# Kernel optimization log

Hardware: AMD Instinct MI355X
Metric: run time of the kernel (lower is better)

## Reference

```python
import jax, jax.numpy as jnp
import numpy as np
from jax import lax

N = 2048
B = 8
CH = 10
START = 1
STOP = 65


def setup_inputs() -> dict:
    key = jax.random.key(0)
    ks = jax.random.split(key, 13)

    def g(k, s):
        return jax.random.normal(k, s, jnp.float32) * 0.05

    return {
        "x": jax.random.normal(ks[0], (B, 1, N, N), jnp.float32),
        "wl": g(ks[1], (CH // 2, 1, 3, N)), "bl": g(ks[2], (CH // 2,)),
        "wr": g(ks[3], (CH // 2, 1, N, 3)), "br": g(ks[4], (CH // 2,)),
        "wA": g(ks[5], (CH, CH, 3)), "bA": g(ks[6], (CH,)),
        "wB": g(ks[7], (CH, CH, 3)), "bB": g(ks[8], (CH,)),  # shared by layers 2&3 (torch list aliasing)
        "wT": g(ks[9], (CH, CH, 3)), "bT": g(ks[10], (CH,)),
        "wm": g(ks[11], (2, CH, 1)), "bm": g(ks[12], (2,)),
        "start": START, "stop": STOP,
    }


def _conv1d(h, w, b, pad):
    y = lax.conv_general_dilated(h, w, (1,), [(pad, pad)], dimension_numbers=("NCH", "OIH", "NCH"))
    return y + b[None, :, None]


def _forward(x, wl, bl, wr, br, wA, bA, wB, bB, wT, bT, wm, bm, start, stop):
    n = x.shape[-1]
    # scan_left: Conv2d kernel (3, n), padding (1, 0) -> (B, 5, n, 1) -> squeeze
    left_ = lax.conv_general_dilated(x, wl, (1, 1), [(1, 1), (0, 0)], dimension_numbers=("NCHW", "OIHW", "NCHW"))
    left_ = left_[..., 0] + bl[None, :, None]
    # scan_right: Conv2d kernel (n, 3), padding (0, 1) -> (B, 5, 1, n) -> squeeze
    right_ = lax.conv_general_dilated(x, wr, (1, 1), [(0, 0), (1, 1)], dimension_numbers=("NCHW", "OIHW", "NCHW"))
    right_ = right_[:, :, 0, :] + br[None, :, None]
    lr = jnp.concatenate([left_, right_], axis=1)  # (B, 10, n)
    h = jax.nn.relu(_conv1d(lr, wA, bA, 1))
    h = jax.nn.relu(_conv1d(h, wB, bB, 1))  # same weights twice: torch [conv, relu]*2 aliasing
    h = jax.nn.relu(_conv1d(h, wB, bB, 1))
    # ConvTranspose1d(k=3, stride=1, pad=1) == Conv1d with transposed, spatially-flipped kernel, pad=1
    wTc = jnp.flip(jnp.swapaxes(wT, 0, 1), -1)
    for _ in range(3):
        h = jax.nn.relu(_conv1d(h, wTc, bT, 1))
    m = jax.nn.sigmoid(_conv1d(h, wm, bm, 0))  # (B, 2, n)
    left, right = m[:, 0, :], m[:, 1, :]
    xs = x[:, 0]  # (B, n, n)
    preds = []
    for d in range(start, stop):  # static diagonal indices
        curr = jnp.exp(jnp.diagonal(xs, offset=d, axis1=1, axis2=2))  # (B, n-d)
        mass_in = curr[:, 1:] * right[:, 1:n - d] + curr[:, :-1] * left[:, d:n - 1]
        mass_out = right[:, 0:n - d - 1] + left[:, d + 1:n]
        p = jnp.log(mass_in / mass_out)
        preds.append(p - jnp.mean(p))  # scalar mean over batch+positions, as torch.mean
    return jnp.concatenate(preds, axis=1)  # ragged preds concatenated: (B, sum(n-d-1))


def reference(x, wl, bl, wr, br, wA, bA, wB, bB, wT, bT, wm, bm, start, stop):
    return _forward(x, wl, bl, wr, br, wA, bA, wB, bB, wT, bT, wm, bm, start, stop)
```

## Files before the change

kernel.cpp:

```cpp
#include <hip/hip_runtime.h>
#include <hip/hip_bf16.h>

#define NN 2048
#define BB 8
#define TROW 128928

typedef __attribute__((ext_vector_type(8))) short bf16x8;
typedef __attribute__((ext_vector_type(4))) float f32x4;

__device__ __forceinline__ short f2bf(float f) {
    unsigned u = __float_as_uint(f);
    unsigned r = (u + 0x7FFFu + ((u >> 16) & 1u)) >> 16;
    return (short)r;
}

__global__ __launch_bounds__(256) void k_leftm(const float* __restrict__ x,
                                               const float* __restrict__ wl,
                                               const float* __restrict__ wr,
                                               float* __restrict__ Rp,
                                               float* __restrict__ WF,
                                               float* __restrict__ psum) {
    if (blockIdx.x == 0 && threadIdx.x < 64) psum[threadIdx.x] = 0.f;
    if (blockIdx.x < 128) {
        int idx = blockIdx.x * 256 + threadIdx.x;
        int h = idx >> 4, k = idx & 15;
        float v = 0.f;
        if (k < 15) {
            int c = k / 3, dw = k - c * 3;
            v = wr[c * (NN * 3) + h * 3 + dw];
        }
        WF[idx] = v;
    }
    int b = blockIdx.x >> 7;
    int sub = blockIdx.x & 127;
    int rg = sub >> 2, ks = sub & 3;
    int wv = threadIdx.x >> 6, lane = threadIdx.x & 63;
    int q = lane >> 4, m = lane & 15;
    int r0 = rg * 64 + wv * 16;
    int nrow = (m == 15) ? 14 : m;
    int k0 = ks * 512 + q * 8;

    const float* ap = x + ((size_t)(b * NN + r0 + m)) * NN + k0;
    const float* bp = wl + (size_t)nrow * NN + k0;

    f32x4 acc = {0.f, 0.f, 0.f, 0.f};
#pragma unroll 4
    for (int it = 0; it < 16; it++) {
        const float* a0 = ap + it * 32;
        const float* b0 = bp + it * 32;
        float4 av0 = *(const float4*)(a0);
        float4 av1 = *(const float4*)(a0 + 4);
        float4 bv0 = *(const float4*)(b0);
        float4 bv1 = *(const float4*)(b0 + 4);
        bf16x8 af, bf;
        af[0] = f2bf(av0.x); af[1] = f2bf(av0.y); af[2] = f2bf(av0.z); af[3] = f2bf(av0.w);
        af[4] = f2bf(av1.x); af[5] = f2bf(av1.y); af[6] = f2bf(av1.z); af[7] = f2bf(av1.w);
        bf[0] = f2bf(bv0.x); bf[1] = f2bf(bv0.y); bf[2] = f2bf(bv0.z); bf[3] = f2bf(bv0.w);
        bf[4] = f2bf(bv1.x); bf[5] = f2bf(bv1.y); bf[6] = f2bf(bv1.z); bf[7] = f2bf(bv1.w);
        acc = __builtin_amdgcn_mfma_f32_16x16x32_bf16(af, bf, acc, 0, 0, 0);
    }
    float* rp = Rp + (size_t)ks * 262144 + ((size_t)b * NN + r0) * 16;
#pragma unroll
    for (int reg = 0; reg < 4; reg++)
        rp[(q * 4 + reg) * 16 + m] = acc[reg];
}

__global__ __launch_bounds__(512) void k_right(const float* __restrict__ x,
                                               const float* __restrict__ WF,
                                               float* __restrict__ CSp) {
    int b = blockIdx.x >> 5;
    int rem = blockIdx.x & 31;
    int jc = rem >> 4, rc = rem & 15;
    int r0 = rc * 128;
    int w = threadIdx.x >> 6, lane = threadIdx.x & 63;
    int c0 = jc * 1024 + w * 128 + lane * 2;
    const float* xp = x + ((size_t)b * NN + r0) * NN + c0;

    float acc[15][2];
#pragma unroll
    for (int k = 0; k < 15; k++) { acc[k][0] = 0.f; acc[k][1] = 0.f; }

    for (int rb = 0; rb < 16; rb++) {
        float2 xv[8];
#pragma unroll
        for (int q = 0; q < 8; q++)
            xv[q] = *(const float2*)(xp + (size_t)(rb * 8 + q) * NN);
#pragma unroll
        for (int q = 0; q < 8; q++) {
            const float* wrow = WF + (size_t)(r0 + rb * 8 + q) * 16;
#pragma unroll
            for (int k = 0; k < 15; k++) {
                float wk = wrow[k];
                acc[k][0] = fmaf(xv[q].x, wk, acc[k][0]);
                acc[k][1] = fmaf(xv[q].y, wk, acc[k][1]);
            }
        }
    }
    float* outp = CSp + ((size_t)(rc * BB + b) * 16) * NN + c0;
#pragma unroll
    for (int k = 0; k < 15; k++) {
        float2 v; v.x = acc[k][0]; v.y = acc[k][1];
        *(float2*)(outp + (size_t)k * NN) = v;
    }
}

__global__ __launch_bounds__(256) void k_csum(const float* __restrict__ CSp,
                                              float* __restrict__ CS,
                                              const float* __restrict__ Rp,
                                              float* __restrict__ R) {
    int blk = blockIdx.x;
    if (blk < 256) {
        int vid = blk * 256 + threadIdx.x;
        const float4* src = (const float4*)CSp;
        float4 s = src[vid];
#pragma unroll
        for (int rc = 1; rc < 16; rc++) {
            float4 v = src[vid + rc * 65536];
            s.x += v.x; s.y += v.y; s.z += v.z; s.w += v.w;
        }
        ((float4*)CS)[vid] = s;
    } else {
        int vid = (blk - 256) * 256 + threadIdx.x;
        const float4* src = (const float4*)Rp;
        float4 s = src[vid];
#pragma unroll
        for (int ks = 1; ks < 4; ks++) {
            float4 v = src[vid + ks * 65536];
            s.x += v.x; s.y += v.y; s.z += v.z; s.w += v.w;
        }
        ((float4*)R)[vid] = s;
    }
}

__global__ __launch_bounds__(256) void k_chainC(const float* __restrict__ R,
                                                const float* __restrict__ CS,
                                                const float* __restrict__ bl,
                                                const float* __restrict__ br,
                                                const float* __restrict__ wA, const float* __restrict__ bA,
                                                const float* __restrict__ wB, const float* __restrict__ bB,
                                                const float* __restrict__ wT, const float* __restrict__ bT,
                                                const float* __restrict__ wm, const float* __restrict__ bm,
                                                float* __restrict__ LEFT, float* __restrict__ RIGHT) {
    __shared__ float buf0[10][144], buf1[10][144];
    __shared__ float W[3][10][10][3];
    __shared__ float Bs[3][10];
    __shared__ float Wm[2][10], Bm[2];
    int b = blockIdx.x >> 4;
    int c0 = (blockIdx.x & 15) << 7;
    int tid = threadIdx.x;

    for (int idx = tid; idx < 900; idx += 256) {
        int set = idx / 300, rem = idx - set * 300;
        int o = rem / 30, rem2 = rem - o * 30, c = rem2 / 3, kk = rem2 - c * 3;
        float u;
        if (set == 0) u = wA[o * 30 + c * 3 + kk];
        else if (set == 1) u = wB[o * 30 + c * 3 + kk];
        else u = wT[c * 30 + o * 3 + (2 - kk)];
        W[set][o][c][kk] = u;
    }
    if (tid < 30) {
        float v = (tid < 10) ? bA[tid] : (tid < 20) ? bB[tid - 10] : bT[tid - 20];
        Bs[tid / 10][tid % 10] = v;
    }
    if (tid < 20) Wm[tid / 10][tid % 10] = wm[tid];
    if (tid < 2) Bm[tid] = bm[tid];

    for (int idx = tid; idx < 1400; idx += 256) {
        int ch = idx / 140, p = idx - ch * 140;
        int g = c0 - 6 + p;
        float v = 0.f;
        if (g >= 0 && g < NN) {
            if (ch < 5) {
                v = bl[ch];
#pragma unroll
                for (int dh = 0; dh < 3; dh++) {
                    int r = g + dh - 1;
                    if (r >= 0 && r < NN) v += R[(size_t)(b * NN + r) * 16 + ch * 3 + dh];
                }
            } else {
                int c = ch - 5;
                v = br[c];
#pragma unroll
                for (int dw = 0; dw < 3; dw++) {
                    int j = g + dw - 1;
                    if (j >= 0 && j < NN)
                        v += CS[((size_t)b * 16 + c * 3 + dw) * NN + j];
                }
            }
        }
        buf0[ch][p] = v;
    }
    __syncthreads();

    float(*in)[144] = buf0;
    float(*out)[144] = buf1;
    for (int layer = 0; layer < 6; layer++) {
        int set = (layer == 0) ? 0 : (layer < 3 ? 1 : 2);
        int lo = layer + 1;
        for (int idx = tid; idx < 1400; idx += 256) {
            int o = idx / 140, p = idx - o * 140;
            if (p >= lo && p < 140 - lo) {
                float s = Bs[set][o];
#pragma unroll
                for (int c = 0; c < 10; c++) {
                    const float* ip = &in[c][p];
                    s = fmaf(ip[-1], W[set][o][c][0], s);
                    s = fmaf(ip[0], W[set][o][c][1], s);
                    s = fmaf(ip[1], W[set][o][c][2], s);
                }
                s = s > 0.f ? s : 0.f;
                int g = c0 - 6 + p;
                if (g < 0 || g >= NN) s = 0.f;
                out[o][p] = s;
            }
        }
        __syncthreads();
        float(*tmp)[144] = in; in = out; out = tmp;
    }
    {
        int idx = tid;
        int o = idx >> 7, pp = idx & 127;
        int p = 6 + pp;
        float s = Bm[o];
#pragma unroll
        for (int c = 0; c < 10; c++) s = fmaf(in[c][p], Wm[o][c], s);
        float sig = 1.f / (1.f + __expf(-s));
        (o ? RIGHT : LEFT)[b * NN + c0 + pp] = sig;
    }
}

__global__ __launch_bounds__(256) void k_diagmass(const float* __restrict__ x,
                                                  const float* __restrict__ LEFT,
                                                  const float* __restrict__ RIGHT,
                                                  float* __restrict__ P,
                                                  float* __restrict__ psum) {
    __shared__ float T[65][65];
    __shared__ float psl[64];
    int b = blockIdx.x >> 5;
    int i0 = (blockIdx.x & 31) << 6;
    int tid = threadIdx.x;

    for (int idx = tid; idx < 65 * 64; idx += 256) {
        int r = idx >> 6, dm1 = idx & 63;
        int row = i0 + r;
        int col = row + dm1 + 1;
        float v = 0.f;
        if (row < NN && col < NN) v = __expf(x[((size_t)b * NN + row) * NN + col]);
        T[r][dm1] = v;
    }
    __syncthreads();

    int wv = tid >> 6, lane = tid & 63;
    int i = i0 + lane;
    const float* lf = LEFT + b * NN;
    const float* rt = RIGHT + b * NN;
#pragma unroll
    for (int s = 0; s < 16; s++) {
        int dm1 = wv * 16 + s;
        int d = dm1 + 1;
        int L = (NN - 1) - d;
        float p = 0.f;
        if (i < L) {
            float mi = T[lane + 1][dm1] * rt[i + 1] + T[lane][dm1] * lf[d + i];
            float mo = rt[i] + lf[d + 1 + i];
            p = __logf(mi / mo);
            P[((size_t)dm1 * BB + b) * NN + i] = p;
        }
        float s64 = p;
        for (int off = 32; off; off >>= 1) s64 += __shfl_down(s64, off);
        if (lane == 0) psl[dm1] = s64;
    }
    __syncthreads();
    if (tid < 64) atomicAdd(&psum[tid], psl[tid]);
}

__global__ __launch_bounds__(1024) void k_out(const float* __restrict__ P,
                                              const float* __restrict__ psum,
                                              float* __restrict__ outp) {
    int dm1 = blockIdx.x >> 2, q = blockIdx.x & 3;
    int d = dm1 + 1;
    int L = (NN - 1) - d;
    int tid = threadIdx.x;
    int b2 = tid >> 9, ii = tid & 511;
    int i = q * 512 + ii;
    if (i >= L) return;
    float mean = psum[dm1] / (float)(8 * L);
    size_t off0 = (size_t)dm1 * (NN - 1) - (size_t)dm1 * (dm1 + 1) / 2;
#pragma unroll
    for (int bs = 0; bs < 4; bs++) {
        int b = b2 + bs * 2;
        outp[(size_t)b * TROW + off0 + i] = P[((size_t)dm1 * BB + b) * NN + i] - mean;
    }
}

extern "C" void kernel_launch(void* const* d_in, const int* in_sizes, int n_in,
                              void* d_out, int out_size, void* d_ws, size_t ws_size,
                              hipStream_t stream) {
    const float* x = (const float*)d_in[0];
    const float* wl = (const float*)d_in[1];
    const float* bl = (const float*)d_in[2];
    const float* wr = (const float*)d_in[3];
    const float* br = (const float*)d_in[4];
    const float* wA = (const float*)d_in[5];
    const float* bA = (const float*)d_in[6];
    const float* wB = (const float*)d_in[7];
    const float* bB = (const float*)d_in[8];
    const float* wT = (const float*)d_in[9];
    const float* bT = (const float*)d_in[10];
    const float* wm = (const float*)d_in[11];
    const float* bm = (const float*)d_in[12];

    float* ws = (float*)d_ws;
    float* R    = ws;
    float* Rp   = ws + 262144;
    float* CSp  = ws + 1310720;
    float* WF   = ws + 5505024;
    float* CS   = ws + 5537792;
    float* LEFT = ws + 5799936;
    float* RIGHT= ws + 5816320;
    float* P    = ws + 5832704;
    float* psum = ws + 6881280;

    k_leftm<<<1024, 256, 0, stream>>>(x, wl, wr, Rp, WF, psum);
    k_right<<<256, 512, 0, stream>>>(x, WF, CSp);
    k_csum<<<512, 256, 0, stream>>>(CSp, CS, Rp, R);
    k_chainC<<<128, 256, 0, stream>>>(R, CS, bl, br, wA, bA, wB, bB, wT, bT, wm, bm, LEFT, RIGHT);
    k_diagmass<<<256, 256, 0, stream>>>(x, LEFT, RIGHT, P, psum);
    k_out<<<256, 1024, 0, stream>>>(P, psum, (float*)d_out);
}
```

Baseline: 305.9 us.

## Fuse left/right scans into one launch and fuse diag-mass with output via grid barrier

```diff
diff --git a/kernel.cpp b/kernel.cpp
--- a/kernel.cpp
+++ b/kernel.cpp
@@ -14,93 +14,92 @@
     return (short)r;
 }
 
-__global__ __launch_bounds__(256) void k_leftm(const float* __restrict__ x,
-                                               const float* __restrict__ wl,
-                                               const float* __restrict__ wr,
-                                               float* __restrict__ Rp,
-                                               float* __restrict__ WF,
-                                               float* __restrict__ psum) {
-    if (blockIdx.x == 0 && threadIdx.x < 64) psum[threadIdx.x] = 0.f;
-    if (blockIdx.x < 128) {
-        int idx = blockIdx.x * 256 + threadIdx.x;
-        int h = idx >> 4, k = idx & 15;
-        float v = 0.f;
-        if (k < 15) {
-            int c = k / 3, dw = k - c * 3;
-            v = wr[c * (NN * 3) + h * 3 + dw];
-        }
-        WF[idx] = v;
-    }
-    int b = blockIdx.x >> 7;
-    int sub = blockIdx.x & 127;
-    int rg = sub >> 2, ks = sub & 3;
-    int wv = threadIdx.x >> 6, lane = threadIdx.x & 63;
-    int q = lane >> 4, m = lane & 15;
-    int r0 = rg * 64 + wv * 16;
-    int nrow = (m == 15) ? 14 : m;
-    int k0 = ks * 512 + q * 8;
-
-    const float* ap = x + ((size_t)(b * NN + r0 + m)) * NN + k0;
-    const float* bp = wl + (size_t)nrow * NN + k0;
-
-    f32x4 acc = {0.f, 0.f, 0.f, 0.f};
+__global__ __launch_bounds__(256) void k_stage1(const float* __restrict__ x,
+                                                const float* __restrict__ wl,
+                                                const float* __restrict__ wr,
+                                                float* __restrict__ Rp,
+                                                float* __restrict__ CSp,
+                                                float* __restrict__ psum,
+                                                int* __restrict__ counter) {
+    int blk = blockIdx.x;
+    int tid = threadIdx.x;
+    if (blk == 0 && tid < 65) {
+        if (tid < 64) psum[tid] = 0.f;
+        else *counter = 0;
+    }
+    if (blk < 1024) {
+        int b = blk >> 7;
+        int sub = blk & 127;
+        int rg = sub >> 2, ks = sub & 3;
+        int wv = tid >> 6, lane = tid & 63;
+        int q = lane >> 4, m = lane & 15;
+        int r0 = rg * 64 + wv * 16;
+        int nrow = (m == 15) ? 14 : m;
+        int k0 = ks * 512 + q * 8;
+
+        const float* ap = x + ((size_t)(b * NN + r0 + m)) * NN + k0;
+        const float* bp = wl + (size_t)nrow * NN + k0;
+
+        f32x4 acc = {0.f, 0.f, 0.f, 0.f};
 #pragma unroll 4
-    for (int it = 0; it < 16; it++) {
-        const float* a0 = ap + it * 32;
-        const float* b0 = bp + it * 32;
-        float4 av0 = *(const float4*)(a0);
-        float4 av1 = *(const float4*)(a0 + 4);
-        float4 bv0 = *(const float4*)(b0);
-        float4 bv1 = *(const float4*)(b0 + 4);
-        bf16x8 af, bf;
-        af[0] = f2bf(av0.x); af[1] = f2bf(av0.y); af[2] = f2bf(av0.z); af[3] = f2bf(av0.w);
-        af[4] = f2bf(av1.x); af[5] = f2bf(av1.y); af[6] = f2bf(av1.z); af[7] = f2bf(av1.w);
-        bf[0] = f2bf(bv0.x); bf[1] = f2bf(bv0.y); bf[2] = f2bf(bv0.z); bf[3] = f2bf(bv0.w);
-        bf[4] = f2bf(bv1.x); bf[5] = f2bf(bv1.y); bf[6] = f2bf(bv1.z); bf[7] = f2bf(bv1.w);
-        acc = __builtin_amdgcn_mfma_f32_16x16x32_bf16(af, bf, acc, 0, 0, 0);
-    }
-    float* rp = Rp + (size_t)ks * 262144 + ((size_t)b * NN + r0) * 16;
-#pragma unroll
-    for (int reg = 0; reg < 4; reg++)
-        rp[(q * 4 + reg) * 16 + m] = acc[reg];
-}
-
-__global__ __launch_bounds__(512) void k_right(const float* __restrict__ x,
-                                               const float* __restrict__ WF,
-                                               float* __restrict__ CSp) {
-    int b = blockIdx.x >> 5;
-    int rem = blockIdx.x & 31;
-    int jc = rem >> 4, rc = rem & 15;
-    int r0 = rc * 128;
-    int w = threadIdx.x >> 6, lane = threadIdx.x & 63;
-    int c0 = jc * 1024 + w * 128 + lane * 2;
-    const float* xp = x + ((size_t)b * NN + r0) * NN + c0;
-
-    float acc[15][2];
-#pragma unroll
-    for (int k = 0; k < 15; k++) { acc[k][0] = 0.f; acc[k][1] = 0.f; }
-
-    for (int rb = 0; rb < 16; rb++) {
-        float2 xv[8];
-#pragma unroll
-        for (int q = 0; q < 8; q++)
-            xv[q] = *(const float2*)(xp + (size_t)(rb * 8 + q) * NN);
-#pragma unroll
-        for (int q = 0; q < 8; q++) {
-            const float* wrow = WF + (size_t)(r0 + rb * 8 + q) * 16;
-#pragma unroll
-            for (int k = 0; k < 15; k++) {
-                float wk = wrow[k];
-                acc[k][0] = fmaf(xv[q].x, wk, acc[k][0]);
-                acc[k][1] = fmaf(xv[q].y, wk, acc[k][1]);
+        for (int it = 0; it < 16; it++) {
+            const float* a0 = ap + it * 32;
+            const float* b0 = bp + it * 32;
+            float4 av0 = *(const float4*)(a0);
+            float4 av1 = *(const float4*)(a0 + 4);
+            float4 bv0 = *(const float4*)(b0);
+            float4 bv1 = *(const float4*)(b0 + 4);
+            bf16x8 af, bf;
+            af[0] = f2bf(av0.x); af[1] = f2bf(av0.y); af[2] = f2bf(av0.z); af[3] = f2bf(av0.w);
+            af[4] = f2bf(av1.x); af[5] = f2bf(av1.y); af[6] = f2bf(av1.z); af[7] = f2bf(av1.w);
+            bf[0] = f2bf(bv0.x); bf[1] = f2bf(bv0.y); bf[2] = f2bf(bv0.z); bf[3] = f2bf(bv0.w);
+            bf[4] = f2bf(bv1.x); bf[5] = f2bf(bv1.y); bf[6] = f2bf(bv1.z); bf[7] = f2bf(bv1.w);
+            acc = __builtin_amdgcn_mfma_f32_16x16x32_bf16(af, bf, acc, 0, 0, 0);
+        }
+        float* rp = Rp + (size_t)ks * 262144 + ((size_t)b * NN + r0) * 16;
+#pragma unroll
+        for (int reg = 0; reg < 4; reg++)
+            rp[(q * 4 + reg) * 16 + m] = acc[reg];
+    } else {
+        int blk2 = blk - 1024;
+        int b = blk2 >> 5;
+        int rem = blk2 & 31;
+        int jc = rem >> 4, rc = rem & 15;
+        int r0 = rc * 128;
+        int c0 = jc * 1024 + tid * 4;
+        const float* xp = x + ((size_t)b * NN + r0) * NN + c0;
+
+        float acc[15][4];
+#pragma unroll
+        for (int k = 0; k < 15; k++)
+#pragma unroll
+            for (int e = 0; e < 4; e++) acc[k][e] = 0.f;
+
+        for (int rb = 0; rb < 16; rb++) {
+            float4 xv[8];
+#pragma unroll
+            for (int q = 0; q < 8; q++)
+                xv[q] = *(const float4*)(xp + (size_t)(rb * 8 + q) * NN);
+#pragma unroll
+            for (int q = 0; q < 8; q++) {
+                int h = r0 + rb * 8 + q;
+#pragma unroll
+                for (int k = 0; k < 15; k++) {
+                    int c = k / 3, dw = k - c * 3;
+                    float wk = wr[c * (NN * 3) + h * 3 + dw];
+                    acc[k][0] = fmaf(xv[q].x, wk, acc[k][0]);
+                    acc[k][1] = fmaf(xv[q].y, wk, acc[k][1]);
+                    acc[k][2] = fmaf(xv[q].z, wk, acc[k][2]);
+                    acc[k][3] = fmaf(xv[q].w, wk, acc[k][3]);
+                }
             }
         }
-    }
-    float* outp = CSp + ((size_t)(rc * BB + b) * 16) * NN + c0;
-#pragma unroll
-    for (int k = 0; k < 15; k++) {
-        float2 v; v.x = acc[k][0]; v.y = acc[k][1];
-        *(float2*)(outp + (size_t)k * NN) = v;
+        float* outp = CSp + ((size_t)(rc * BB + b) * 16) * NN + c0;
+#pragma unroll
+        for (int k = 0; k < 15; k++) {
+            float4 v; v.x = acc[k][0]; v.y = acc[k][1]; v.z = acc[k][2]; v.w = acc[k][3];
+            *(float4*)(outp + (size_t)k * NN) = v;
+        }
     }
 }
 
@@ -229,11 +228,12 @@
     }
 }
 
-__global__ __launch_bounds__(256) void k_diagmass(const float* __restrict__ x,
-                                                  const float* __restrict__ LEFT,
-                                                  const float* __restrict__ RIGHT,
-                                                  float* __restrict__ P,
-                                                  float* __restrict__ psum) {
+__global__ __launch_bounds__(256) void k_diagout(const float* __restrict__ x,
+                                                 const float* __restrict__ LEFT,
+                                                 const float* __restrict__ RIGHT,
+                                                 float* __restrict__ psum,
+                                                 int* __restrict__ counter,
+                                                 float* __restrict__ outp) {
     __shared__ float T[65][65];
     __shared__ float psl[64];
     int b = blockIdx.x >> 5;
@@ -254,6 +254,7 @@
     int i = i0 + lane;
     const float* lf = LEFT + b * NN;
     const float* rt = RIGHT + b * NN;
+    float pv[16];
 #pragma unroll
     for (int s = 0; s < 16; s++) {
         int dm1 = wv * 16 + s;
@@ -264,32 +265,35 @@
             float mi = T[lane + 1][dm1] * rt[i + 1] + T[lane][dm1] * lf[d + i];
             float mo = rt[i] + lf[d + 1 + i];
             p = __logf(mi / mo);
-            P[((size_t)dm1 * BB + b) * NN + i] = p;
-        }
+        }
+        pv[s] = p;
         float s64 = p;
         for (int off = 32; off; off >>= 1) s64 += __shfl_down(s64, off);
         if (lane == 0) psl[dm1] = s64;
     }
     __syncthreads();
     if (tid < 64) atomicAdd(&psum[tid], psl[tid]);
-}
-
-__global__ __launch_bounds__(1024) void k_out(const float* __restrict__ P,
-                                              const float* __restrict__ psum,
-                                              float* __restrict__ outp) {
-    int dm1 = blockIdx.x >> 2, q = blockIdx.x & 3;
-    int d = dm1 + 1;
-    int L = (NN - 1) - d;
-    int tid = threadIdx.x;
-    int b2 = tid >> 9, ii = tid & 511;
-    int i = q * 512 + ii;
-    if (i >= L) return;
-    float mean = psum[dm1] / (float)(8 * L);
-    size_t off0 = (size_t)dm1 * (NN - 1) - (size_t)dm1 * (dm1 + 1) / 2;
-#pragma unroll
-    for (int bs = 0; bs < 4; bs++) {
-        int b = b2 + bs * 2;
-        outp[(size_t)b * TROW + off0 + i] = P[((size_t)dm1 * BB + b) * NN + i] - mean;
+    __syncthreads();
+    if (tid == 0) {
+        __threadfence();
+        atomicAdd(counter, 1);
+        while (__hip_atomic_load(counter, __ATOMIC_ACQUIRE, __HIP_MEMORY_SCOPE_AGENT) < 256) {}
+    }
+    __syncthreads();
+    if (tid < 64)
+        psl[tid] = __hip_atomic_load(&psum[tid], __ATOMIC_RELAXED, __HIP_MEMORY_SCOPE_AGENT);
+    __syncthreads();
+
+#pragma unroll
+    for (int s = 0; s < 16; s++) {
+        int dm1 = wv * 16 + s;
+        int d = dm1 + 1;
+        int L = (NN - 1) - d;
+        if (i < L) {
+            float mean = psl[dm1] / (float)(8 * L);
+            size_t off0 = (size_t)dm1 * (NN - 1) - (size_t)dm1 * (dm1 + 1) / 2;
+            outp[(size_t)b * TROW + off0 + i] = pv[s] - mean;
+        }
     }
 }
 
@@ -314,17 +318,14 @@
     float* R    = ws;
     float* Rp   = ws + 262144;
     float* CSp  = ws + 1310720;
-    float* WF   = ws + 5505024;
-    float* CS   = ws + 5537792;
-    float* LEFT = ws + 5799936;
-    float* RIGHT= ws + 5816320;
-    float* P    = ws + 5832704;
-    float* psum = ws + 6881280;
-
-    k_leftm<<<1024, 256, 0, stream>>>(x, wl, wr, Rp, WF, psum);
-    k_right<<<256, 512, 0, stream>>>(x, WF, CSp);
+    float* CS   = ws + 5505024;
+    float* LEFT = ws + 5767168;
+    float* RIGHT= ws + 5783552;
+    float* psum = ws + 5799936;
+    int*   counter = (int*)(ws + 5800000);
+
+    k_stage1<<<1280, 256, 0, stream>>>(x, wl, wr, Rp, CSp, psum, counter);
     k_csum<<<512, 256, 0, stream>>>(CSp, CS, Rp, R);
     k_chainC<<<128, 256, 0, stream>>>(R, CS, bl, br, wA, bA, wB, bB, wT, bT, wm, bm, LEFT, RIGHT);
-    k_diagmass<<<256, 256, 0, stream>>>(x, LEFT, RIGHT, P, psum);
-    k_out<<<256, 1024, 0, stream>>>(P, psum, (float*)d_out);
-}
+    k_diagout<<<256, 256, 0, stream>>>(x, LEFT, RIGHT, psum, counter, (float*)d_out);
+}
```

Measured after the change: 296.0 us. -3.2%, faster.
